# Performance work log

Measured on AMD Instinct MI355X. Metric: run time of the kernel, lower is better.

## Reference

```python
import jax, jax.numpy as jnp
import numpy as np

DIM = 1024
HEADS = 16
DK = DIM // HEADS
B, LQ, LKV = 2, 2048, 2048


def setup_inputs() -> dict:
    key = jax.random.key(0)
    ks = jax.random.split(key, 12)
    s = 1.0 / np.sqrt(DIM)
    return {
        "output": jax.random.normal(ks[0], (B, LQ, DIM), jnp.float32),
        "context": jax.random.normal(ks[1], (B, LKV, DIM), jnp.float32),
        # torch nn.Linear(dim, dim): store as [in, out] so y = x @ W + b
        "Wq": jax.random.normal(ks[2], (DIM, DIM), jnp.float32) * s,
        "bq": jax.random.normal(ks[3], (DIM,), jnp.float32) * s,
        "Wk": jax.random.normal(ks[4], (DIM, DIM), jnp.float32) * s,
        "bk": jax.random.normal(ks[5], (DIM,), jnp.float32) * s,
        "Wv": jax.random.normal(ks[6], (DIM, DIM), jnp.float32) * s,
        "bv": jax.random.normal(ks[7], (DIM,), jnp.float32) * s,
        # linear_out: in = 2*dim, out = dim
        "Wo": jax.random.normal(ks[8], (2 * DIM, DIM), jnp.float32) * (1.0 / np.sqrt(2 * DIM)),
        "bo": jax.random.normal(ks[9], (DIM,), jnp.float32) * (1.0 / np.sqrt(2 * DIM)),
    }


def _to_batches(x):
    # [B, L, dim] -> [B*H, L, dk], same layout as the torch reshape/permute
    b, l, _ = x.shape
    return x.reshape(b, l, HEADS, DK).transpose(0, 2, 1, 3).reshape(b * HEADS, l, DK)


def reference(output, context, Wq, bq, Wk, bk, Wv, bv, Wo, bo):
    b, lq, dim = output.shape
    q = _to_batches(output @ Wq + bq)     # [B*H, Lq, dk]
    k = _to_batches(context @ Wk + bk)    # [B*H, Lkv, dk]
    v = _to_batches(context @ Wv + bv)    # [B*H, Lkv, dk]

    scores = jnp.einsum('bqd,bkd->bqk', q, k) / jnp.sqrt(jnp.asarray(DK, q.dtype))
    attn = jax.nn.softmax(scores, axis=-1)            # [B*H, Lq, Lkv]; dropout = identity at eval
    ctx = jnp.einsum('bqk,bkd->bqd', attn, v)          # [B*H, Lq, dk]

    # Faithful to the original (non-standard) reshape:
    # scores.transpose(1,2).contiguous().view(B, -1, dim)
    concat = ctx.transpose(0, 2, 1).reshape(b, -1, dim)  # [B, Lq, dim] (permuted layout)
    combined = jnp.concatenate([concat, output], axis=2)  # [B, Lq, 2*dim]
    out = jnp.tanh(combined @ Wo + bo)                     # [B, Lq, dim]
    return (out, attn)
```

## Files before the change

kernel.cpp:

```cpp
#include <hip/hip_runtime.h>
#include <math.h>
#include <stdint.h>

#define DIM_ 1024
#define HEADS_ 16
#define DK_ 64
#define B_ 2
#define L_ 2048
#define BH_ (B_*HEADS_)
#define M_ (B_*L_)

typedef __attribute__((ext_vector_type(4))) float f32x4;
typedef __attribute__((ext_vector_type(8))) short bf16x8;
typedef __attribute__((ext_vector_type(4))) short bf16x4;

#define QSCALE 0.18033688f

static __device__ __forceinline__ short f2bf(float f) {
    uint32_t u = __builtin_bit_cast(uint32_t, f);
    u += 0x7fffu + ((u >> 16) & 1u);
    return (short)(u >> 16);
}
static __device__ __forceinline__ float bf2f(short h) {
    uint32_t u = ((uint32_t)(unsigned short)h) << 16;
    return __builtin_bit_cast(float, u);
}
static __device__ __forceinline__ void gload16(const void* g, void* l) {
    __builtin_amdgcn_global_load_lds(
        (const __attribute__((address_space(1))) unsigned int*)g,
        (__attribute__((address_space(3))) unsigned int*)l, 16, 0, 0);
}

__global__ __launch_bounds__(256)
void cvt_bf16(const float* __restrict__ a, const float* __restrict__ b,
              short* __restrict__ ao, short* __restrict__ bo)
{
    const int id = blockIdx.x * 256 + threadIdx.x;
    const int nA = (M_ * DIM_) / 8;
    const float* src = (id < nA) ? a : b;
    short* dst = (id < nA) ? ao : bo;
    const int c = (id < nA) ? id : id - nA;
    const f32x4 v0 = *(const f32x4*)&src[(size_t)c * 8];
    const f32x4 v1 = *(const f32x4*)&src[(size_t)c * 8 + 4];
    bf16x8 o;
#pragma unroll
    for (int i = 0; i < 4; ++i) { o[i] = f2bf(v0[i]); o[4 + i] = f2bf(v1[i]); }
    *(bf16x8*)&dst[(size_t)c * 8] = o;
}

__global__ __launch_bounds__(256)
void wtrans(const float* __restrict__ Wq, const float* __restrict__ Wk,
            const float* __restrict__ Wv, const float* __restrict__ Wo,
            short* __restrict__ WqT, short* __restrict__ WkT,
            short* __restrict__ WvT, short* __restrict__ WoT)
{
    const int z = blockIdx.z;
    const int K = (z == 3) ? 2 * DIM_ : DIM_;
    const int k0 = blockIdx.x * 64;
    if (k0 >= K) return;
    const int n0 = blockIdx.y * 64;
    const float* W = (z == 0) ? Wq : (z == 1) ? Wk : (z == 2) ? Wv : Wo;
    short* WT = (z == 0) ? WqT : (z == 1) ? WkT : (z == 2) ? WvT : WoT;

    __shared__ float ts[64][65];
    const int tid = threadIdx.x;
    {
        const int k = tid >> 2, noff = (tid & 3) * 16;
#pragma unroll
        for (int i = 0; i < 4; ++i)
            *(f32x4*)&ts[k][noff + i * 4] =
                *(const f32x4*)&W[(size_t)(k0 + k) * DIM_ + n0 + noff + i * 4];
    }
    __syncthreads();
    {
        const int n = tid >> 2, koff = (tid & 3) * 16;
#pragma unroll
        for (int c = 0; c < 2; ++c) {
            bf16x8 o;
#pragma unroll
            for (int i = 0; i < 8; ++i) o[i] = f2bf(ts[koff + c * 8 + i][n]);
            *(bf16x8*)&WT[(size_t)(n0 + n) * K + k0 + koff + c * 8] = o;
        }
    }
}

__global__ __launch_bounds__(256)
void qkv_mfma(const short* __restrict__ xoutb, const short* __restrict__ xctxb,
              const short* __restrict__ WqT, const short* __restrict__ WkT,
              const short* __restrict__ WvT,
              const float* __restrict__ bq, const float* __restrict__ bk,
              const float* __restrict__ bv,
              short* __restrict__ qh, short* __restrict__ kh, short* __restrict__ vT)
{
    const int z = blockIdx.z;
    const short* A  = (z == 0) ? xoutb : xctxb;
    const short* Bt = (z == 0) ? WqT : (z == 1) ? WkT : WvT;
    const float* bias = (z == 0) ? bq : (z == 1) ? bk : bv;

    const int flat = blockIdx.y * 8 + blockIdx.x;
    const int wgs = (flat & 7) * 32 + (flat >> 3);
    const int col0 = (wgs & 7) * 128;
    const int row0 = (wgs >> 3) * 128;
    const int tid = threadIdx.x;
    const int lane = tid & 63;
    const int w = tid >> 6;
    const int wm = (w >> 1) * 64, wn = (w & 1) * 64;
    const int l15 = lane & 15, g = lane >> 4;
    const int sub = lane >> 3, slt = lane & 7;

    __shared__ short As[128 * 64];
    __shared__ short Bs[128 * 64];

    const short* pA[4]; const short* pB[4]; short* ldsA[4]; short* ldsB[4];
#pragma unroll
    for (int i = 0; i < 4; ++i) {
        const int r = w * 32 + i * 8 + sub;
        const int sc = ((slt ^ (r & 7)) * 8);
        pA[i] = A  + (size_t)(row0 + r) * DIM_ + sc;
        pB[i] = Bt + (size_t)(col0 + r) * DIM_ + sc;
        ldsA[i] = &As[(w * 32 + i * 8) * 64];
        ldsB[i] = &Bs[(w * 32 + i * 8) * 64];
    }

    f32x4 acc[4][4];
#pragma unroll
    for (int mi = 0; mi < 4; ++mi)
#pragma unroll
        for (int ni = 0; ni < 4; ++ni) acc[mi][ni] = (f32x4)0.f;

    for (int k0 = 0; k0 < DIM_; k0 += 64) {
#pragma unroll
        for (int i = 0; i < 4; ++i) {
            gload16(pA[i] + k0, ldsA[i]);
            gload16(pB[i] + k0, ldsB[i]);
        }
        __syncthreads();
        bf16x8 af[4][2], bfr[4][2];
#pragma unroll
        for (int mi = 0; mi < 4; ++mi) {
            const int wa = wm + mi * 16 + l15;
#pragma unroll
            for (int ks = 0; ks < 2; ++ks)
                af[mi][ks] = *(const bf16x8*)&As[wa * 64 + (((ks * 4 + g) ^ (wa & 7)) * 8)];
        }
#pragma unroll
        for (int ni = 0; ni < 4; ++ni) {
            const int wb = wn + ni * 16 + l15;
#pragma unroll
            for (int ks = 0; ks < 2; ++ks)
                bfr[ni][ks] = *(const bf16x8*)&Bs[wb * 64 + (((ks * 4 + g) ^ (wb & 7)) * 8)];
        }
        __builtin_amdgcn_s_setprio(1);
#pragma unroll
        for (int mi = 0; mi < 4; ++mi)
#pragma unroll
            for (int ni = 0; ni < 4; ++ni)
#pragma unroll
                for (int ks = 0; ks < 2; ++ks)
                    acc[mi][ni] = __builtin_amdgcn_mfma_f32_16x16x32_bf16(af[mi][ks], bfr[ni][ks], acc[mi][ni], 0, 0, 0);
        __builtin_amdgcn_s_setprio(0);
        __syncthreads();
    }

#pragma unroll
    for (int ni = 0; ni < 4; ++ni) {
        const int col = col0 + wn + ni * 16 + l15;
        const int h = col >> 6, dk = col & 63;
        const float bb = bias[col];
#pragma unroll
        for (int mi = 0; mi < 4; ++mi) {
            const int rowb = row0 + wm + mi * 16 + g * 4;
            const int b = rowb >> 11;
            const int l = rowb & (L_ - 1);
            const int bh = b * 16 + h;
            if (z == 2) {
                bf16x4 o;
#pragma unroll
                for (int r = 0; r < 4; ++r) o[r] = f2bf(acc[mi][ni][r] + bb);
                *(bf16x4*)&vT[(size_t)(bh * 64 + dk) * L_ + l] = o;
            } else {
                short* dst = (z == 0) ? qh : kh;
                const float sc = (z == 0) ? QSCALE : 1.0f;
#pragma unroll
                for (int r = 0; r < 4; ++r)
                    dst[((size_t)bh * L_ + l + r) * DK_ + dk] = f2bf((acc[mi][ni][r] + bb) * sc);
            }
        }
    }
}

__global__ __launch_bounds__(512, 8)
void attn_mfma(const short* __restrict__ qh, const short* __restrict__ kh,
               const short* __restrict__ vT,
               float* __restrict__ attn, short* __restrict__ ctxTb)
{
    const int bid = blockIdx.x;
    const int wg = (bid & 7) * 128 + (bid >> 3);
    const int bh = wg >> 5;
    const int q0 = (wg & 31) * 64;

    const int tid = threadIdx.x;
    const int lane = tid & 63;
    const int w = tid >> 6;
    const int wq = w >> 1, wk = w & 1;
    const int l15 = lane & 15, g = lane >> 4;

    __shared__ short Kb0[64 * 64];
    __shared__ short Kb1[64 * 64];
    __shared__ short Vb[64 * 64];
    __shared__ short Psb[64 * 72];
    __shared__ float stat[4][2][16][2];

    const short* kbase = kh + (size_t)bh * (L_ * DK_);
    const short* vbase = vT + (size_t)bh * (DK_ * L_);

    const int lr = lane >> 3, ls = lane & 7;
    const int srow = w * 8 + lr;
    const short* kSrc = kbase + (size_t)srow * DK_ + ((ls ^ (srow & 7)) * 8);
    const short* vSrc = vbase + (size_t)srow * L_ + ((ls ^ (srow & 7)) * 8);
    short* kDst0 = &Kb0[w * 512];
    short* kDst1 = &Kb1[w * 512];
    short* vDst  = &Vb[w * 512];

    bf16x8 qf[2];
#pragma unroll
    for (int ks = 0; ks < 2; ++ks)
        qf[ks] = *(const bf16x8*)&qh[((size_t)bh * L_ + q0 + wq * 16 + l15) * DK_ + ks * 32 + g * 8];

    int kbOff[2][2], vbOff[4];
#pragma unroll
    for (int cc = 0; cc < 2; ++cc)
#pragma unroll
        for (int ks = 0; ks < 2; ++ks) {
            const int row = wk * 32 + cc * 16 + l15;
            kbOff[cc][ks] = row * 64 + (((ks * 4 + g) ^ (row & 7)) * 8);
        }
#pragma unroll
    for (int nf = 0; nf < 4; ++nf) {
        const int row = nf * 16 + l15;
        vbOff[nf] = row * 64 + (((wk * 4 + g) ^ (row & 7)) * 8);
    }

    float m[4], s[4];
#pragma unroll
    for (int r = 0; r < 4; ++r) { m[r] = -1e30f; s[r] = 0.f; }

    gload16(kSrc, kDst0);
    asm volatile("s_waitcnt vmcnt(0)" ::: "memory");
    __builtin_amdgcn_sched_barrier(0);
    __builtin_amdgcn_s_barrier();
    for (int t = 0; t < 32; ++t) {
        if (t) {
            asm volatile("s_waitcnt vmcnt(0)" ::: "memory");
            __builtin_amdgcn_sched_barrier(0);
            __builtin_amdgcn_s_barrier();
        }
        if (t < 31) gload16(kSrc + (size_t)(t + 1) * 64 * DK_, (t & 1) ? kDst0 : kDst1);
        const short* kb = (t & 1) ? Kb1 : Kb0;
        f32x4 sa[2];
#pragma unroll
        for (int cc = 0; cc < 2; ++cc) sa[cc] = (f32x4)0.f;
        __builtin_amdgcn_s_setprio(1);
#pragma unroll
        for (int cc = 0; cc < 2; ++cc)
#pragma unroll
            for (int ks = 0; ks < 2; ++ks)
                sa[cc] = __builtin_amdgcn_mfma_f32_16x16x32_bf16(qf[ks], *(const bf16x8*)&kb[kbOff[cc][ks]], sa[cc], 0, 0, 0);
        __builtin_amdgcn_s_setprio(0);
#pragma unroll
        for (int r = 0; r < 4; ++r) {
            const float tm = fmaxf(sa[0][r], sa[1][r]);
            const float mn = fmaxf(m[r], tm);
            s[r] = s[r] * exp2f(m[r] - mn) + exp2f(sa[0][r] - mn) + exp2f(sa[1][r] - mn);
            m[r] = mn;
        }
    }
#pragma unroll
    for (int mask = 1; mask <= 8; mask <<= 1) {
#pragma unroll
        for (int r = 0; r < 4; ++r) {
            const float mo = __shfl_xor(m[r], mask);
            const float so = __shfl_xor(s[r], mask);
            const float mn = fmaxf(m[r], mo);
            s[r] = s[r] * exp2f(m[r] - mn) + so * exp2f(mo - mn);
            m[r] = mn;
        }
    }
    if (l15 == 0) {
#pragma unroll
        for (int r = 0; r < 4; ++r) {
            stat[wq][wk][g * 4 + r][0] = m[r];
            stat[wq][wk][g * 4 + r][1] = s[r];
        }
    }
    gload16(kSrc, kDst0);
    asm volatile("s_waitcnt lgkmcnt(0)" ::: "memory");
    __builtin_amdgcn_s_barrier();
    float inv_s[4];
#pragma unroll
    for (int r = 0; r < 4; ++r) {
        const float m0 = stat[wq][0][g * 4 + r][0], s0 = stat[wq][0][g * 4 + r][1];
        const float m1 = stat[wq][1][g * 4 + r][0], s1 = stat[wq][1][g * 4 + r][1];
        const float mn = fmaxf(m0, m1);
        m[r] = mn;
        inv_s[r] = 1.0f / (s0 * exp2f(m0 - mn) + s1 * exp2f(m1 - mn));
    }

    f32x4 cacc[4];
#pragma unroll
    for (int nf = 0; nf < 4; ++nf) cacc[nf] = (f32x4)0.f;

    float* attnB = attn + ((size_t)bh * L_ + q0) * L_;

    asm volatile("s_waitcnt vmcnt(0)" ::: "memory");
    __builtin_amdgcn_sched_barrier(0);
    __builtin_amdgcn_s_barrier();

    for (int t = 0; t < 32; ++t) {
        if (t) {
            asm volatile("s_waitcnt vmcnt(8)" ::: "memory");
            __builtin_amdgcn_sched_barrier(0);
            __builtin_amdgcn_s_barrier();
        }
        gload16(vSrc + t * 64, vDst);
        {
            const int tn = (t < 31) ? t + 1 : t;
            gload16(kSrc + (size_t)tn * 64 * DK_, (t & 1) ? kDst0 : kDst1);
        }
        const short* kb = (t & 1) ? Kb1 : Kb0;
        f32x4 sa[2];
#pragma unroll
        for (int cc = 0; cc < 2; ++cc) sa[cc] = (f32x4)0.f;
        __builtin_amdgcn_s_setprio(1);
#pragma unroll
        for (int cc = 0; cc < 2; ++cc)
#pragma unroll
            for (int ks = 0; ks < 2; ++ks)
                sa[cc] = __builtin_amdgcn_mfma_f32_16x16x32_bf16(qf[ks], *(const bf16x8*)&kb[kbOff[cc][ks]], sa[cc], 0, 0, 0);
        __builtin_amdgcn_s_setprio(0);
#pragma unroll
        for (int cc = 0; cc < 2; ++cc)
#pragma unroll
            for (int r = 0; r < 4; ++r) {
                const float p = exp2f(sa[cc][r] - m[r]) * inv_s[r];
                Psb[(wq * 16 + g * 4 + r) * 72 + wk * 32 + cc * 16 + l15] = f2bf(p);
                __builtin_nontemporal_store(
                    p, attnB + (size_t)(wq * 16 + g * 4 + r) * L_ + t * 64 + wk * 32 + cc * 16 + l15);
            }
        asm volatile("s_waitcnt vmcnt(9) lgkmcnt(0)" ::: "memory");
        __builtin_amdgcn_sched_barrier(0);
        __builtin_amdgcn_s_barrier();
        const bf16x8 pa = *(const bf16x8*)&Psb[(wq * 16 + l15) * 72 + wk * 32 + g * 8];
        __builtin_amdgcn_s_setprio(1);
#pragma unroll
        for (int nf = 0; nf < 4; ++nf)
            cacc[nf] = __builtin_amdgcn_mfma_f32_16x16x32_bf16(pa, *(const bf16x8*)&Vb[vbOff[nf]], cacc[nf], 0, 0, 0);
        __builtin_amdgcn_s_setprio(0);
    }

    __syncthreads();
    float* scr = (float*)&Kb0[0];
    float* scr1 = (float*)&Kb1[0];
    if (wk) {
#pragma unroll
        for (int nf = 0; nf < 4; ++nf) {
            float* p = (nf < 2) ? scr : scr1;
            *(f32x4*)&p[(((wq * 2) + (nf & 1)) * 64 + lane) * 4] = cacc[nf];
        }
    }
    __syncthreads();
    if (!wk) {
#pragma unroll
        for (int nf = 0; nf < 4; ++nf) {
            const float* p = (nf < 2) ? scr : scr1;
            const f32x4 o = cacc[nf] + *(const f32x4*)&p[(((wq * 2) + (nf & 1)) * 64 + lane) * 4];
            bf16x4 ob;
#pragma unroll
            for (int r = 0; r < 4; ++r) ob[r] = f2bf(o[r]);
            *(bf16x4*)&ctxTb[(size_t)(bh * 64 + nf * 16 + l15) * L_ + q0 + wq * 16 + g * 4] = ob;
        }
    }
}

__global__ __launch_bounds__(256)
void out_mfma(const short* __restrict__ ctxTb, const short* __restrict__ xoutb,
              const short* __restrict__ WoT, const float* __restrict__ bo,
              float* __restrict__ out)
{
    const int flat = blockIdx.y * 16 + blockIdx.x;
    const int wgs = (flat & 7) * 64 + (flat >> 3);
    const int col0 = (wgs & 15) * 64;
    const int row0 = (wgs >> 4) * 128;
    const int tid = threadIdx.x;
    const int lane = tid & 63;
    const int w = tid >> 6;
    const int wm = (w >> 1) * 64, wn = (w & 1) * 32;
    const int l15 = lane & 15, g = lane >> 4;
    const int sub = lane >> 3, slt = lane & 7;

    __shared__ short As[128 * 64];
    __shared__ short Bs[64 * 64];

    const short* pA1[4]; const short* pA2[4]; const short* pB[2];
    short* ldsA[4]; short* ldsB[2];
#pragma unroll
    for (int i = 0; i < 4; ++i) {
        const int r = w * 32 + i * 8 + sub;
        const int rr = row0 + r;
        const int b = rr >> 11, l_ = rr & (L_ - 1);
        const int bh = b * 16 + (l_ >> 7), d = (l_ & 127) >> 1;
        const size_t off1 = ((size_t)(bh * 64 + d) << 11) + (size_t)((l_ & 1) << 10);
        const int sc = ((slt ^ (r & 7)) * 8);
        pA1[i] = ctxTb + off1 + sc;
        pA2[i] = xoutb + (size_t)rr * DIM_ + sc;
        ldsA[i] = &As[(w * 32 + i * 8) * 64];
    }
#pragma unroll
    for (int i = 0; i < 2; ++i) {
        const int r = w * 16 + i * 8 + sub;
        const int sc = ((slt ^ (r & 7)) * 8);
        pB[i]  = WoT + (size_t)(col0 + r) * (2 * DIM_) + sc;
        ldsB[i] = &Bs[(w * 16 + i * 8) * 64];
    }

    f32x4 acc[4][2];
#pragma unroll
    for (int mi = 0; mi < 4; ++mi)
#pragma unroll
        for (int ni = 0; ni < 2; ++ni) acc[mi][ni] = (f32x4)0.f;

    for (int k0 = 0; k0 < 2 * DIM_; k0 += 64) {
        const bool first = (k0 < DIM_);
        const int kk = first ? k0 : k0 - DIM_;
#pragma unroll
        for (int i = 0; i < 4; ++i)
            gload16(first ? (pA1[i] + kk) : (pA2[i] + kk), ldsA[i]);
#pragma unroll
        for (int i = 0; i < 2; ++i)
            gload16(pB[i] + k0, ldsB[i]);
        __syncthreads();
        bf16x8 af[4][2], bfr[2][2];
#pragma unroll
        for (int mi = 0; mi < 4; ++mi) {
            const int wa = wm + mi * 16 + l15;
#pragma unroll
            for (int ks = 0; ks < 2; ++ks)
                af[mi][ks] = *(const bf16x8*)&As[wa * 64 + (((ks * 4 + g) ^ (wa & 7)) * 8)];
        }
#pragma unroll
        for (int ni = 0; ni < 2; ++ni) {
            const int wb = wn + ni * 16 + l15;
#pragma unroll
            for (int ks = 0; ks < 2; ++ks)
                bfr[ni][ks] = *(const bf16x8*)&Bs[wb * 64 + (((ks * 4 + g) ^ (wb & 7)) * 8)];
        }
        __builtin_amdgcn_s_setprio(1);
#pragma unroll
        for (int mi = 0; mi < 4; ++mi)
#pragma unroll
            for (int ni = 0; ni < 2; ++ni)
#pragma unroll
                for (int ks = 0; ks < 2; ++ks)
                    acc[mi][ni] = __builtin_amdgcn_mfma_f32_16x16x32_bf16(af[mi][ks], bfr[ni][ks], acc[mi][ni], 0, 0, 0);
        __builtin_amdgcn_s_setprio(0);
        __syncthreads();
    }

#pragma unroll
    for (int ni = 0; ni < 2; ++ni) {
        const int col = col0 + wn + ni * 16 + l15;
        const float bb = bo[col];
#pragma unroll
        for (int mi = 0; mi < 4; ++mi) {
            const int rowb = row0 + wm + mi * 16 + g * 4;
#pragma unroll
            for (int r = 0; r < 4; ++r)
                out[(size_t)(rowb + r) * DIM_ + col] = tanhf(acc[mi][ni][r] + bb);
        }
    }
}

extern "C" void kernel_launch(void* const* d_in, const int* in_sizes, int n_in,
                              void* d_out, int out_size, void* d_ws, size_t ws_size,
                              hipStream_t stream)
{
    const float* xout = (const float*)d_in[0];
    const float* xctx = (const float*)d_in[1];
    const float* Wq = (const float*)d_in[2];
    const float* bq = (const float*)d_in[3];
    const float* Wk = (const float*)d_in[4];
    const float* bk = (const float*)d_in[5];
    const float* Wv = (const float*)d_in[6];
    const float* bv = (const float*)d_in[7];
    const float* Wo = (const float*)d_in[8];
    const float* bo = (const float*)d_in[9];

    float* out  = (float*)d_out;
    float* attn = out + (size_t)M_ * DIM_;

    short* ws = (short*)d_ws;
    short* xoutb = ws;
    short* xctxb = xoutb + (size_t)M_ * DIM_;
    short* WqT   = xctxb + (size_t)M_ * DIM_;
    short* WkT   = WqT + (size_t)DIM_ * DIM_;
    short* WvT   = WkT + (size_t)DIM_ * DIM_;
    short* WoT   = WvT + (size_t)DIM_ * DIM_;
    short* qh    = WoT + (size_t)2 * DIM_ * DIM_;
    short* kh    = qh + (size_t)BH_ * L_ * DK_;
    short* vT    = kh + (size_t)BH_ * L_ * DK_;
    short* ctxTb = vT + (size_t)BH_ * L_ * DK_;

    cvt_bf16<<<(2 * M_ * DIM_ / 8) / 256, 256, 0, stream>>>(xout, xctx, xoutb, xctxb);
    wtrans<<<dim3(32, 16, 4), 256, 0, stream>>>(Wq, Wk, Wv, Wo, WqT, WkT, WvT, WoT);
    qkv_mfma<<<dim3(8, 32, 3), 256, 0, stream>>>(
        xoutb, xctxb, WqT, WkT, WvT, bq, bk, bv, qh, kh, vT);
    attn_mfma<<<1024, 512, 0, stream>>>(qh, kh, vT, attn, ctxTb);
    out_mfma<<<dim3(16, 32), 256, 0, stream>>>(ctxTb, xoutb, WoT, bo, out);
}
```

Baseline: 283.7 us.

## Split softmax row-statistics pass into a separate register-blocked kernel

Moves the first attention pass (row max and sum of exponentials over all keys) out of the fused attention kernel into a new attn_stats kernel. The new kernel handles 128 queries per 256-thread block and loads K fragments straight from global memory into registers, with no LDS staging and no barriers. It writes per-row max and inverse sum to workspace, which the PV kernel then reads. This trades an extra launch and a small workspace round trip for a barrier-free stats pass with more reuse of each K fragment and a simpler PV kernel.

```diff
diff --git a/kernel.cpp b/kernel.cpp
--- a/kernel.cpp
+++ b/kernel.cpp
@@ -20,10 +20,6 @@
     uint32_t u = __builtin_bit_cast(uint32_t, f);
     u += 0x7fffu + ((u >> 16) & 1u);
     return (short)(u >> 16);
-}
-static __device__ __forceinline__ float bf2f(short h) {
-    uint32_t u = ((uint32_t)(unsigned short)h) << 16;
-    return __builtin_bit_cast(float, u);
 }
 static __device__ __forceinline__ void gload16(const void* g, void* l) {
     __builtin_amdgcn_global_load_lds(
@@ -189,10 +185,93 @@
     }
 }
 
+__global__ __launch_bounds__(256, 4)
+void attn_stats(const short* __restrict__ qh, const short* __restrict__ kh,
+                float* __restrict__ mws, float* __restrict__ isws)
+{
+    const int bid = blockIdx.x;
+    const int wg = (bid & 7) * 64 + (bid >> 3);
+    const int bh = wg >> 4;
+    const int q0 = (wg & 15) * 128;
+    const int tid = threadIdx.x;
+    const int lane = tid & 63;
+    const int w = tid >> 6;
+    const int l15 = lane & 15, g = lane >> 4;
+
+    const short* kbase = kh + (size_t)bh * (L_ * DK_);
+
+    bf16x8 qf[2][2];
+#pragma unroll
+    for (int u = 0; u < 2; ++u)
+#pragma unroll
+        for (int ks = 0; ks < 2; ++ks)
+            qf[u][ks] = *(const bf16x8*)&qh[((size_t)bh * L_ + q0 + w * 32 + u * 16 + l15) * DK_ + ks * 32 + g * 8];
+
+    float m[2][4], s[2][4];
+#pragma unroll
+    for (int u = 0; u < 2; ++u)
+#pragma unroll
+        for (int r = 0; r < 4; ++r) { m[u][r] = -1e30f; s[u][r] = 0.f; }
+
+    for (int t = 0; t < 32; ++t) {
+        const short* kt = kbase + (size_t)t * 64 * DK_;
+        bf16x8 kf[4][2];
+#pragma unroll
+        for (int cc = 0; cc < 4; ++cc)
+#pragma unroll
+            for (int ks = 0; ks < 2; ++ks)
+                kf[cc][ks] = *(const bf16x8*)&kt[(size_t)(cc * 16 + l15) * DK_ + ks * 32 + g * 8];
+#pragma unroll
+        for (int u = 0; u < 2; ++u) {
+            f32x4 sa[4];
+#pragma unroll
+            for (int cc = 0; cc < 4; ++cc) sa[cc] = (f32x4)0.f;
+#pragma unroll
+            for (int cc = 0; cc < 4; ++cc)
+#pragma unroll
+                for (int ks = 0; ks < 2; ++ks)
+                    sa[cc] = __builtin_amdgcn_mfma_f32_16x16x32_bf16(qf[u][ks], kf[cc][ks], sa[cc], 0, 0, 0);
+#pragma unroll
+            for (int r = 0; r < 4; ++r) {
+                const float tm = fmaxf(fmaxf(sa[0][r], sa[1][r]), fmaxf(sa[2][r], sa[3][r]));
+                const float mn = fmaxf(m[u][r], tm);
+                s[u][r] = s[u][r] * exp2f(m[u][r] - mn)
+                        + exp2f(sa[0][r] - mn) + exp2f(sa[1][r] - mn)
+                        + exp2f(sa[2][r] - mn) + exp2f(sa[3][r] - mn);
+                m[u][r] = mn;
+            }
+        }
+    }
+#pragma unroll
+    for (int mask = 1; mask <= 8; mask <<= 1) {
+#pragma unroll
+        for (int u = 0; u < 2; ++u)
+#pragma unroll
+            for (int r = 0; r < 4; ++r) {
+                const float mo = __shfl_xor(m[u][r], mask);
+                const float so = __shfl_xor(s[u][r], mask);
+                const float mn = fmaxf(m[u][r], mo);
+                s[u][r] = s[u][r] * exp2f(m[u][r] - mn) + so * exp2f(mo - mn);
+                m[u][r] = mn;
+            }
+    }
+    if (l15 == 0) {
+#pragma unroll
+        for (int u = 0; u < 2; ++u)
+#pragma unroll
+            for (int r = 0; r < 4; ++r) {
+                const int row = bh * L_ + q0 + w * 32 + u * 16 + g * 4 + r;
+                mws[row]  = m[u][r];
+                isws[row] = 1.0f / s[u][r];
+            }
+    }
+}
+
 __global__ __launch_bounds__(512, 8)
-void attn_mfma(const short* __restrict__ qh, const short* __restrict__ kh,
-               const short* __restrict__ vT,
-               float* __restrict__ attn, short* __restrict__ ctxTb)
+void attn_pv(const short* __restrict__ qh, const short* __restrict__ kh,
+             const short* __restrict__ vT,
+             const float* __restrict__ mws, const float* __restrict__ isws,
+             float* __restrict__ attn, short* __restrict__ ctxTb)
 {
     const int bid = blockIdx.x;
     const int wg = (bid & 7) * 128 + (bid >> 3);
@@ -209,7 +288,6 @@
     __shared__ short Kb1[64 * 64];
     __shared__ short Vb[64 * 64];
     __shared__ short Psb[64 * 72];
-    __shared__ float stat[4][2][16][2];
 
     const short* kbase = kh + (size_t)bh * (L_ * DK_);
     const short* vbase = vT + (size_t)bh * (DK_ * L_);
@@ -227,6 +305,14 @@
     for (int ks = 0; ks < 2; ++ks)
         qf[ks] = *(const bf16x8*)&qh[((size_t)bh * L_ + q0 + wq * 16 + l15) * DK_ + ks * 32 + g * 8];
 
+    float m[4], inv_s[4];
+#pragma unroll
+    for (int r = 0; r < 4; ++r) {
+        const int row = bh * L_ + q0 + wq * 16 + g * 4 + r;
+        m[r] = mws[row];
+        inv_s[r] = isws[row];
+    }
+
     int kbOff[2][2], vbOff[4];
 #pragma unroll
     for (int cc = 0; cc < 2; ++cc)
@@ -241,77 +327,13 @@
         vbOff[nf] = row * 64 + (((wk * 4 + g) ^ (row & 7)) * 8);
     }
 
-    float m[4], s[4];
-#pragma unroll
-    for (int r = 0; r < 4; ++r) { m[r] = -1e30f; s[r] = 0.f; }
+    f32x4 cacc[4];
+#pragma unroll
+    for (int nf = 0; nf < 4; ++nf) cacc[nf] = (f32x4)0.f;
+
+    float* attnB = attn + ((size_t)bh * L_ + q0) * L_;
 
     gload16(kSrc, kDst0);
-    asm volatile("s_waitcnt vmcnt(0)" ::: "memory");
-    __builtin_amdgcn_sched_barrier(0);
-    __builtin_amdgcn_s_barrier();
-    for (int t = 0; t < 32; ++t) {
-        if (t) {
-            asm volatile("s_waitcnt vmcnt(0)" ::: "memory");
-            __builtin_amdgcn_sched_barrier(0);
-            __builtin_amdgcn_s_barrier();
-        }
-        if (t < 31) gload16(kSrc + (size_t)(t + 1) * 64 * DK_, (t & 1) ? kDst0 : kDst1);
-        const short* kb = (t & 1) ? Kb1 : Kb0;
-        f32x4 sa[2];
-#pragma unroll
-        for (int cc = 0; cc < 2; ++cc) sa[cc] = (f32x4)0.f;
-        __builtin_amdgcn_s_setprio(1);
-#pragma unroll
-        for (int cc = 0; cc < 2; ++cc)
-#pragma unroll
-            for (int ks = 0; ks < 2; ++ks)
-                sa[cc] = __builtin_amdgcn_mfma_f32_16x16x32_bf16(qf[ks], *(const bf16x8*)&kb[kbOff[cc][ks]], sa[cc], 0, 0, 0);
-        __builtin_amdgcn_s_setprio(0);
-#pragma unroll
-        for (int r = 0; r < 4; ++r) {
-            const float tm = fmaxf(sa[0][r], sa[1][r]);
-            const float mn = fmaxf(m[r], tm);
-            s[r] = s[r] * exp2f(m[r] - mn) + exp2f(sa[0][r] - mn) + exp2f(sa[1][r] - mn);
-            m[r] = mn;
-        }
-    }
-#pragma unroll
-    for (int mask = 1; mask <= 8; mask <<= 1) {
-#pragma unroll
-        for (int r = 0; r < 4; ++r) {
-            const float mo = __shfl_xor(m[r], mask);
-            const float so = __shfl_xor(s[r], mask);
-            const float mn = fmaxf(m[r], mo);
-            s[r] = s[r] * exp2f(m[r] - mn) + so * exp2f(mo - mn);
-            m[r] = mn;
-        }
-    }
-    if (l15 == 0) {
-#pragma unroll
-        for (int r = 0; r < 4; ++r) {
-            stat[wq][wk][g * 4 + r][0] = m[r];
-            stat[wq][wk][g * 4 + r][1] = s[r];
-        }
-    }
-    gload16(kSrc, kDst0);
-    asm volatile("s_waitcnt lgkmcnt(0)" ::: "memory");
-    __builtin_amdgcn_s_barrier();
-    float inv_s[4];
-#pragma unroll
-    for (int r = 0; r < 4; ++r) {
-        const float m0 = stat[wq][0][g * 4 + r][0], s0 = stat[wq][0][g * 4 + r][1];
-        const float m1 = stat[wq][1][g * 4 + r][0], s1 = stat[wq][1][g * 4 + r][1];
-        const float mn = fmaxf(m0, m1);
-        m[r] = mn;
-        inv_s[r] = 1.0f / (s0 * exp2f(m0 - mn) + s1 * exp2f(m1 - mn));
-    }
-
-    f32x4 cacc[4];
-#pragma unroll
-    for (int nf = 0; nf < 4; ++nf) cacc[nf] = (f32x4)0.f;
-
-    float* attnB = attn + ((size_t)bh * L_ + q0) * L_;
-
     asm volatile("s_waitcnt vmcnt(0)" ::: "memory");
     __builtin_amdgcn_sched_barrier(0);
     __builtin_amdgcn_s_barrier();
@@ -509,11 +531,14 @@
     short* kh    = qh + (size_t)BH_ * L_ * DK_;
     short* vT    = kh + (size_t)BH_ * L_ * DK_;
     short* ctxTb = vT + (size_t)BH_ * L_ * DK_;
+    float* mws   = (float*)(ctxTb + (size_t)BH_ * L_ * DK_);
+    float* isws  = mws + (size_t)BH_ * L_;
 
     cvt_bf16<<<(2 * M_ * DIM_ / 8) / 256, 256, 0, stream>>>(xout, xctx, xoutb, xctxb);
     wtrans<<<dim3(32, 16, 4), 256, 0, stream>>>(Wq, Wk, Wv, Wo, WqT, WkT, WvT, WoT);
     qkv_mfma<<<dim3(8, 32, 3), 256, 0, stream>>>(
         xoutb, xctxb, WqT, WkT, WvT, bq, bk, bv, qh, kh, vT);
-    attn_mfma<<<1024, 512, 0, stream>>>(qh, kh, vT, attn, ctxTb);
+    attn_stats<<<512, 256, 0, stream>>>(qh, kh, mws, isws);
+    attn_pv<<<1024, 512, 0, stream>>>(qh, kh, vT, mws, isws, attn, ctxTb);
     out_mfma<<<dim3(16, 32), 256, 0, stream>>>(ctxTb, xoutb, WoT, bo, out);
 }
```

Result: slower. 344.1 us (+21.3%).
